# Optimization experiments

Hardware: AMD Instinct MI355X
Metric: run time of the kernel (lower is better)

Reference implementation:

```python
import jax, jax.numpy as jnp
import numpy as np

VOCAB = 1_000_000
B, F, E = 16384, 39, 16
LAYERS = [200, 200, 200]


def setup_inputs() -> dict:
    key = jax.random.key(0)
    ks = jax.random.split(key, 12)
    feat_ids = jax.random.randint(ks[0], (B, F), 0, VOCAB)
    feat_vals = jnp.ones((B, F), dtype=jnp.float32)
    # xavier-ish init for tables and MLP weights
    w = jax.random.normal(ks[1], (VOCAB, 1), dtype=jnp.float32) * 0.01
    v = jax.random.normal(ks[2], (VOCAB, E), dtype=jnp.float32) * 0.01
    b = jnp.zeros((1,), dtype=jnp.float32)
    params = {}
    node_in = E
    for i, h in enumerate(LAYERS):
        scale = (2.0 / (node_in + h)) ** 0.5
        params[f'w{i}'] = jax.random.normal(ks[3 + i], (node_in, h), dtype=jnp.float32) * scale
        params[f'b{i}'] = jnp.zeros((h,), dtype=jnp.float32)
        node_in = h
    return dict(feat_ids=feat_ids, feat_vals=feat_vals, w=w, v=v, b=b,
                w0=params['w0'], b0=params['b0'],
                w1=params['w1'], b1=params['b1'],
                w2=params['w2'], b2=params['b2'])


def reference(feat_ids, feat_vals, w, v, b, w0, b0, w1, b1, w2, b2):
    # X @ v  (sparse one-hot matmul == embedding gather + weighted sum over fields)
    ve = v[feat_ids]                                   # [B, F, E]
    xv = jnp.einsum('bf,bfe->be', feat_vals, ve)       # [B, E]
    # X^2 @ v^2
    x2v2 = jnp.einsum('bf,bfe->be', feat_vals * feat_vals, ve * ve)  # [B, E]
    fm = 0.5 * (xv * xv - x2v2)                        # [B, E]
    # MLP (dropout in test mode: keep_prob = 1 -> identity)
    h = jax.nn.relu(fm @ w0 + b0)
    h = jax.nn.relu(h @ w1 + b1)
    h = jax.nn.relu(h @ w2 + b2)
    bilinear = jnp.sum(h, axis=1, keepdims=True)       # [B, 1]
    # LR part: X @ w
    lr = jnp.einsum('bf,bfo->bo', feat_vals, w[feat_ids])  # [B, 1]
    logits = jnp.reshape(lr + b + bilinear, (-1,))     # [B]
    return jax.nn.sigmoid(logits)
```

## Files before the change

kernel.cpp:

```cpp
#include <hip/hip_runtime.h>
#include <math.h>

#define NFM_B 16384
#define NFM_F 39
#define NFM_E 16
#define NFM_H 200
#define TR    16
#define KPAD  232
#define NT    13

typedef short short8  __attribute__((ext_vector_type(8)));
typedef float floatx4 __attribute__((ext_vector_type(4)));

__device__ __forceinline__ short f2bf(float x) {
    union { float f; unsigned u; } a; a.f = x;
    unsigned r = a.u + 0x7FFF + ((a.u >> 16) & 1);
    return (short)(r >> 16);
}

#define W0F_OFF 0
#define W0F_SZ  (NT * 1 * 64 * 8)
#define W1F_OFF (W0F_OFF + W0F_SZ)
#define W1F_SZ  (NT * 7 * 64 * 8)
#define W2F_OFF (W1F_OFF + W1F_SZ)
#define W2F_SZ  (NT * 7 * 64 * 8)
#define WS_TOTAL (W2F_OFF + W2F_SZ)

__global__ __launch_bounds__(256)
void nfm_prep_kernel(const float* __restrict__ w0,
                     const float* __restrict__ w1,
                     const float* __restrict__ w2,
                     short* __restrict__ ws)
{
    const int idx = blockIdx.x * 256 + threadIdx.x;
    if (idx >= WS_TOTAL) return;
    float val;
    if (idx < W1F_OFF) {
        const int rem = idx;
        const int j = rem & 7, lane = (rem >> 3) & 63, tile = rem >> 9;
        const int k = (lane >> 4) * 8 + j;
        const int n = tile * 16 + (lane & 15);
        val = (k < NFM_E && n < NFM_H) ? w0[k * NFM_H + n] : 0.f;
    } else if (idx < W2F_OFF) {
        const int rem = idx - W1F_OFF;
        const int j = rem & 7, lane = (rem >> 3) & 63;
        const int kt = rem >> 9;
        const int ks = kt % 7, tile = kt / 7;
        const int k = ks * 32 + (lane >> 4) * 8 + j;
        const int n = tile * 16 + (lane & 15);
        val = (k < NFM_H && n < NFM_H) ? w1[k * NFM_H + n] : 0.f;
    } else {
        const int rem = idx - W2F_OFF;
        const int j = rem & 7, lane = (rem >> 3) & 63;
        const int kt = rem >> 9;
        const int ks = kt % 7, tile = kt / 7;
        const int k = ks * 32 + (lane >> 4) * 8 + j;
        const int n = tile * 16 + (lane & 15);
        val = (k < NFM_H && n < NFM_H) ? w2[k * NFM_H + n] : 0.f;
    }
    ws[idx] = f2bf(val);
}

__global__ __launch_bounds__(256, 4)
void nfm_main_kernel(
    const int*   __restrict__ feat_ids,
    const float* __restrict__ feat_vals,
    const float* __restrict__ w,
    const float* __restrict__ v,
    const float* __restrict__ bglob,
    const float* __restrict__ b0,
    const float* __restrict__ b1,
    const float* __restrict__ b2,
    const short* __restrict__ ws,
    float* __restrict__ out)
{
    __shared__ __attribute__((aligned(16))) short hbfA[TR * KPAD];
    __shared__ __attribute__((aligned(16))) short hbfB[TR * KPAD];
    __shared__ int   idsS [TR * NFM_F];
    __shared__ float valsS[TR * NFM_F];
    __shared__ float rowsumW[4][TR];
    __shared__ float lrS[TR];

    const int tid  = threadIdx.x;
    const int row0 = blockIdx.x * TR;
    const int lane = tid & 63;
    const int wv   = tid >> 6;
    const int lq   = lane >> 4;
    const int ln   = lane & 15;

    for (int i = tid; i < 2 * TR * 32; i += 256) {
        const int buf = i >> 9;
        const int j   = i & 511;
        const int r   = j >> 5, c = j & 31;
        (buf ? hbfB : hbfA)[r * KPAD + NFM_H + c] = 0;
    }
    for (int i = tid; i < TR * NFM_F; i += 256) {
        idsS [i] = feat_ids [row0 * NFM_F + i];
        valsS[i] = feat_vals[row0 * NFM_F + i];
    }
    __syncthreads();

    {
        const int lane_e = tid & 15;
        const int r      = tid >> 4;
        const int*   ids = idsS  + r * NFM_F;
        const float* vls = valsS + r * NFM_F;
        float xv = 0.f, x2v2 = 0.f;
        for (int f = 0; f < NFM_F; ++f) {
            float ve = v[ids[f] * NFM_E + lane_e];
            float t  = vls[f] * ve;
            xv += t; x2v2 += t * t;
        }
        const float fm = 0.5f * (xv * xv - x2v2);
        hbfB[r * KPAD + lane_e]      = f2bf(fm);
        hbfB[r * KPAD + 16 + lane_e] = 0;
        float lr = 0.f;
        for (int f = lane_e; f < NFM_F; f += 16)
            lr += vls[f] * w[ids[f]];
#pragma unroll
        for (int off = 8; off >= 1; off >>= 1)
            lr += __shfl_xor(lr, off, 16);
        if (lane_e == 0) lrS[r] = lr;
    }
    __syncthreads();

    {
        const short8 af = *(const short8*)&hbfB[ln * KPAD + lq * 8];
        const short* Wf = ws + W0F_OFF;
        for (int t = wv; t < NT; t += 4) {
            const int n = t * 16 + ln;
            const float bj = (n < NFM_H) ? b0[n] : 0.f;
            floatx4 acc = {bj, bj, bj, bj};
            const short8 bf = *(const short8*)&Wf[(t * 64 + lane) * 8];
            acc = __builtin_amdgcn_mfma_f32_16x16x32_bf16(af, bf, acc, 0, 0, 0);
#pragma unroll
            for (int rg = 0; rg < 4; ++rg)
                hbfA[(lq * 4 + rg) * KPAD + n] = f2bf(fmaxf(acc[rg], 0.f));
        }
    }
    __syncthreads();

    {
        short8 af[7];
#pragma unroll
        for (int ks = 0; ks < 7; ++ks)
            af[ks] = *(const short8*)&hbfA[ln * KPAD + ks * 32 + lq * 8];
        const short* Wf = ws + W1F_OFF;
        for (int t = wv; t < NT; t += 4) {
            const int n = t * 16 + ln;
            const float bj = (n < NFM_H) ? b1[n] : 0.f;
            floatx4 acc = {bj, bj, bj, bj};
#pragma unroll
            for (int ks = 0; ks < 7; ++ks) {
                const short8 bf = *(const short8*)&Wf[((t * 7 + ks) * 64 + lane) * 8];
                acc = __builtin_amdgcn_mfma_f32_16x16x32_bf16(af[ks], bf, acc, 0, 0, 0);
            }
#pragma unroll
            for (int rg = 0; rg < 4; ++rg)
                hbfB[(lq * 4 + rg) * KPAD + n] = f2bf(fmaxf(acc[rg], 0.f));
        }
    }
    __syncthreads();

    {
        short8 af[7];
#pragma unroll
        for (int ks = 0; ks < 7; ++ks)
            af[ks] = *(const short8*)&hbfB[ln * KPAD + ks * 32 + lq * 8];
        const short* Wf = ws + W2F_OFF;
        float rs[4] = {0.f, 0.f, 0.f, 0.f};
        for (int t = wv; t < NT; t += 4) {
            const int n = t * 16 + ln;
            const float bj = (n < NFM_H) ? b2[n] : 0.f;
            floatx4 acc = {bj, bj, bj, bj};
#pragma unroll
            for (int ks = 0; ks < 7; ++ks) {
                const short8 bf = *(const short8*)&Wf[((t * 7 + ks) * 64 + lane) * 8];
                acc = __builtin_amdgcn_mfma_f32_16x16x32_bf16(af[ks], bf, acc, 0, 0, 0);
            }
#pragma unroll
            for (int rg = 0; rg < 4; ++rg)
                rs[rg] += fmaxf(acc[rg], 0.f);
        }
#pragma unroll
        for (int off = 8; off >= 1; off >>= 1)
#pragma unroll
            for (int rg = 0; rg < 4; ++rg)
                rs[rg] += __shfl_xor(rs[rg], off, 16);
        if (ln == 0)
#pragma unroll
            for (int rg = 0; rg < 4; ++rg)
                rowsumW[wv][lq * 4 + rg] = rs[rg];
    }
    __syncthreads();

    if (tid < TR) {
        const float s = rowsumW[0][tid] + rowsumW[1][tid]
                      + rowsumW[2][tid] + rowsumW[3][tid];
        const float logit = lrS[tid] + bglob[0] + s;
        out[row0 + tid] = 1.f / (1.f + expf(-logit));
    }
}

extern "C" void kernel_launch(void* const* d_in, const int* in_sizes, int n_in,
                              void* d_out, int out_size, void* d_ws, size_t ws_size,
                              hipStream_t stream) {
    const int*   feat_ids  = (const int*)  d_in[0];
    const float* feat_vals = (const float*)d_in[1];
    const float* w   = (const float*)d_in[2];
    const float* v   = (const float*)d_in[3];
    const float* b   = (const float*)d_in[4];
    const float* w0  = (const float*)d_in[5];
    const float* b0  = (const float*)d_in[6];
    const float* w1  = (const float*)d_in[7];
    const float* b1  = (const float*)d_in[8];
    const float* w2  = (const float*)d_in[9];
    const float* b2  = (const float*)d_in[10];
    float* out = (float*)d_out;
    short* ws  = (short*)d_ws;

    hipLaunchKernelGGL(nfm_prep_kernel, dim3((WS_TOTAL + 255) / 256), dim3(256),
                       0, stream, w0, w1, w2, ws);
    hipLaunchKernelGGL(nfm_main_kernel, dim3(NFM_B / TR), dim3(256), 0, stream,
                       feat_ids, feat_vals, w, v, b, b0, b1, b2, ws, out);
}
```

Baseline: 141.2 us.

## Halve rows per block and vectorize embedding gather with field-split lanes

Cuts rows per block from 16 to 8, doubling the number of blocks, and raises the occupancy hint in launch bounds. The FM gather now has 32 lanes per row, each loading float4 slices of the embedding for a strided subset of fields, then combines them with shuffle reductions; the LR sum is reduced the same way. This targets latency in the random embedding gather by putting more independent loads in flight. In exchange, the MFMA layers still work on 16-row tiles with the upper 8 rows zero-padded, which wastes half the MLP compute, and each block rereads the bf16 weights twice as often per useful row.

New measurement: 152.5 us. 1.08x slower.

```diff
diff --git a/kernel.cpp b/kernel.cpp
--- a/kernel.cpp
+++ b/kernel.cpp
@@ -3,13 +3,15 @@
 
 #define NFM_B 16384
 #define NFM_F 39
+#define NFM_FP 40
 #define NFM_E 16
 #define NFM_H 200
-#define TR    16
+#define TR    8
 #define KPAD  232
 #define NT    13
 
 typedef short short8  __attribute__((ext_vector_type(8)));
+typedef short short4_t __attribute__((ext_vector_type(4)));
 typedef float floatx4 __attribute__((ext_vector_type(4)));
 
 __device__ __forceinline__ short f2bf(float x) {
@@ -61,7 +63,7 @@
     ws[idx] = f2bf(val);
 }
 
-__global__ __launch_bounds__(256, 4)
+__global__ __launch_bounds__(256, 6)
 void nfm_main_kernel(
     const int*   __restrict__ feat_ids,
     const float* __restrict__ feat_vals,
@@ -74,11 +76,11 @@
     const short* __restrict__ ws,
     float* __restrict__ out)
 {
-    __shared__ __attribute__((aligned(16))) short hbfA[TR * KPAD];
-    __shared__ __attribute__((aligned(16))) short hbfB[TR * KPAD];
-    __shared__ int   idsS [TR * NFM_F];
-    __shared__ float valsS[TR * NFM_F];
-    __shared__ float rowsumW[4][TR];
+    __shared__ __attribute__((aligned(16))) short hbfA[16 * KPAD];
+    __shared__ __attribute__((aligned(16))) short hbfB[16 * KPAD];
+    __shared__ int   idsS [TR * NFM_FP];
+    __shared__ float valsS[TR * NFM_FP];
+    __shared__ float rowsumW[4][16];
     __shared__ float lrS[TR];
 
     const int tid  = threadIdx.x;
@@ -88,39 +90,63 @@
     const int lq   = lane >> 4;
     const int ln   = lane & 15;
 
-    for (int i = tid; i < 2 * TR * 32; i += 256) {
-        const int buf = i >> 9;
-        const int j   = i & 511;
-        const int r   = j >> 5, c = j & 31;
-        (buf ? hbfB : hbfA)[r * KPAD + NFM_H + c] = 0;
-    }
-    for (int i = tid; i < TR * NFM_F; i += 256) {
-        idsS [i] = feat_ids [row0 * NFM_F + i];
-        valsS[i] = feat_vals[row0 * NFM_F + i];
-    }
-    __syncthreads();
-
-    {
-        const int lane_e = tid & 15;
-        const int r      = tid >> 4;
-        const int*   ids = idsS  + r * NFM_F;
-        const float* vls = valsS + r * NFM_F;
-        float xv = 0.f, x2v2 = 0.f;
-        for (int f = 0; f < NFM_F; ++f) {
-            float ve = v[ids[f] * NFM_E + lane_e];
-            float t  = vls[f] * ve;
-            xv += t; x2v2 += t * t;
-        }
-        const float fm = 0.5f * (xv * xv - x2v2);
-        hbfB[r * KPAD + lane_e]      = f2bf(fm);
-        hbfB[r * KPAD + 16 + lane_e] = 0;
-        float lr = 0.f;
-        for (int f = lane_e; f < NFM_F; f += 16)
-            lr += vls[f] * w[ids[f]];
-#pragma unroll
-        for (int off = 8; off >= 1; off >>= 1)
-            lr += __shfl_xor(lr, off, 16);
-        if (lane_e == 0) lrS[r] = lr;
+    {
+        short8 z8 = {0, 0, 0, 0, 0, 0, 0, 0};
+        short8* pA = (short8*)hbfA;
+        short8* pB = (short8*)hbfB;
+        for (int i = tid; i < 464; i += 256) { pA[i] = z8; pB[i] = z8; }
+    }
+    for (int i = tid; i < TR * NFM_FP; i += 256) {
+        const int r = i / NFM_FP, f = i - r * NFM_FP;
+        if (f < NFM_F) {
+            idsS [i] = feat_ids [(row0 + r) * NFM_F + f];
+            valsS[i] = feat_vals[(row0 + r) * NFM_F + f];
+        } else {
+            idsS[i] = 0; valsS[i] = 0.f;
+        }
+    }
+    __syncthreads();
+
+    {
+        const int r8  = tid >> 5;
+        const int l32 = tid & 31;
+        const int fs  = l32 >> 2, eg = l32 & 3;
+        const int*   ids = idsS  + r8 * NFM_FP;
+        const float* vls = valsS + r8 * NFM_FP;
+
+        floatx4 xv = {0.f, 0.f, 0.f, 0.f}, x2 = {0.f, 0.f, 0.f, 0.f};
+#pragma unroll
+        for (int it = 0; it < 5; ++it) {
+            const int f = fs + it * 8;
+            const float val = vls[f];
+            const float4 ve = *(const float4*)&v[ids[f] * NFM_E + eg * 4];
+            const float t0 = val * ve.x, t1 = val * ve.y;
+            const float t2 = val * ve.z, t3 = val * ve.w;
+            xv[0] += t0; xv[1] += t1; xv[2] += t2; xv[3] += t3;
+            x2[0] = fmaf(t0, t0, x2[0]); x2[1] = fmaf(t1, t1, x2[1]);
+            x2[2] = fmaf(t2, t2, x2[2]); x2[3] = fmaf(t3, t3, x2[3]);
+        }
+#pragma unroll
+        for (int off = 4; off <= 16; off <<= 1) {
+#pragma unroll
+            for (int c = 0; c < 4; ++c) {
+                xv[c] += __shfl_xor(xv[c], off, 32);
+                x2[c] += __shfl_xor(x2[c], off, 32);
+            }
+        }
+        if (fs == 0) {
+            short4_t fm4;
+#pragma unroll
+            for (int c = 0; c < 4; ++c)
+                fm4[c] = f2bf(0.5f * (xv[c] * xv[c] - x2[c]));
+            *(short4_t*)&hbfB[r8 * KPAD + eg * 4] = fm4;
+        }
+        float lr = vls[l32] * w[ids[l32]];
+        if (l32 < 8) lr += vls[32 + l32] * w[ids[32 + l32]];
+#pragma unroll
+        for (int off = 16; off >= 1; off >>= 1)
+            lr += __shfl_xor(lr, off, 32);
+        if (l32 == 0) lrS[r8] = lr;
     }
     __syncthreads();
 
```
